# Kernel tuning notes

Hardware: AMD Instinct MI355X
Metric: run time of the kernel (lower is better)

The kernel has to match this reference:

```python
import jax, jax.numpy as jnp
import numpy as np

EMB = 1024
HEADS = 16
HEAD = EMB // HEADS
B, S = 4, 1024


def setup_inputs() -> dict:
    key = jax.random.key(0)
    ks = jax.random.split(key, 8)
    glorot = lambda k, shp: jax.random.normal(k, shp, jnp.float32) * np.sqrt(2.0 / (shp[-2] + shp[-1]))
    return {
        "inputs_for_keys": jax.random.normal(ks[0], (B, S, EMB), jnp.float32),
        "inputs_for_values": jax.random.normal(ks[1], (B, S, EMB), jnp.float32),
        "inputs_for_queries": jax.random.normal(ks[2], (B, S, EMB), jnp.float32),
        "Wk": glorot(ks[3], (HEADS, EMB, HEAD)),
        "Wv": glorot(ks[4], (HEADS, EMB, HEAD)),
        "Wq": glorot(ks[5], (HEADS, EMB, HEAD)),
        "Wo": glorot(ks[6], (EMB, EMB)),
        "bo": jnp.zeros((EMB,), jnp.float32),
    }


def reference(inputs_for_keys, inputs_for_values, inputs_for_queries, Wk, Wv, Wq, Wo, bo):
    # Batched equivalent of the per-head loop: project all heads at once.
    K = jnp.einsum("bse,hed->bhsd", inputs_for_keys, Wk)
    V = jnp.einsum("bse,hed->bhsd", inputs_for_values, Wv)
    Q = jnp.einsum("bse,hed->bhsd", inputs_for_queries, Wq)
    s_keys = K.shape[2]
    s_q = Q.shape[2]
    # causal mask: -inf strictly above diagonal (original: np.triu(ones*-inf, k=1))
    mask = jnp.where(jnp.triu(jnp.ones((s_q, s_keys), bool), k=1), -jnp.inf, 0.0).astype(jnp.float32)
    logits = jnp.einsum("bhqd,bhkd->bhqk", Q, K)
    # FAITHFUL quirk: original divides (logits + mask) by sqrt(window_size_keys)
    scores = jax.nn.softmax((logits + mask) / np.sqrt(s_keys), axis=-1)
    ctx = jnp.einsum("bhqk,bhkd->bhqd", scores, V)  # [B,H,Sq,Dh]
    # concat heads along last dim (head order matches loop order)
    concat = ctx.transpose(0, 2, 1, 3).reshape(ctx.shape[0], s_q, -1)  # [B,Sq,E]
    return jax.nn.relu(concat @ Wo + bo)
```

## Files before the change

### kernel.cpp

```cpp
#include <hip/hip_runtime.h>
#include <hip/hip_bf16.h>

typedef unsigned short u16;
typedef unsigned int   u32;
typedef __attribute__((ext_vector_type(4))) float f32x4;
typedef __attribute__((ext_vector_type(8))) short bf16x8;
typedef __attribute__((ext_vector_type(4))) short bf16x4;

#define EMB   1024
#define SEQ   1024
#define HEADS 16
#define DH    64
#define BATCH 4
#define BH    64
#define BS    4096
#define LDP   72
#define NEG_BIG (-1.0e30f)

__device__ __forceinline__ float b2f(u16 u){ return __uint_as_float(((u32)u) << 16); }
__device__ __forceinline__ u16 f2b(float f){
    u32 u = __float_as_uint(f);
    u32 r = u + 0x7fffu + ((u >> 16) & 1u);
    return (u16)(r >> 16);
}
__device__ __forceinline__ void zero4(f32x4& v){ v[0]=0.f; v[1]=0.f; v[2]=0.f; v[3]=0.f; }
__device__ __forceinline__ ushort4 pk4(float a, float b, float c, float d){
    ushort4 p; p.x = f2b(a); p.y = f2b(b); p.z = f2b(c); p.w = f2b(d); return p;
}
__device__ __forceinline__ float exp2g(float x){ return __builtin_amdgcn_exp2f(x); }

__device__ __forceinline__ void gld_lds16(const void* g, void* l){
    __builtin_amdgcn_global_load_lds(
        (const __attribute__((address_space(1))) u32*)g,
        (__attribute__((address_space(3))) u32*)l, 16, 0, 0);
}

__device__ __forceinline__ u16* tptr(u16* base, int row, int col ){
    const int phys = ((col >> 3) ^ (row & 7));
    return base + row * 64 + (phys << 3);
}
__device__ __forceinline__ const u16* tptrc(const u16* base, int row, int col ){
    const int phys = ((col >> 3) ^ (row & 7));
    return base + row * 64 + (phys << 3);
}
__device__ __forceinline__ const u16* tptr8c(const u16* base, int row, int col ){
    const int chunk = ((col >> 3) ^ (row & 7));
    return base + row * 64 + (chunk << 3) + (col & 7);
}

__device__ __forceinline__ void dot2_f32(const float* __restrict__ x,
                                         const float* __restrict__ w, const int ws,
                                         float& a0, float& a1)
{
    float s0 = 0.f, s1 = 0.f;
    for (int e = 0; e < EMB; e += 4) {
        const float4 xv = *(const float4*)(x + e);
        const float2 w0 = *(const float2*)(w + (size_t)(e + 0) * ws);
        const float2 w1 = *(const float2*)(w + (size_t)(e + 1) * ws);
        const float2 w2 = *(const float2*)(w + (size_t)(e + 2) * ws);
        const float2 w3 = *(const float2*)(w + (size_t)(e + 3) * ws);
        s0 += xv.x * w0.x; s1 += xv.x * w0.y;
        s0 += xv.y * w1.x; s1 += xv.y * w1.y;
        s0 += xv.z * w2.x; s1 += xv.z * w2.y;
        s0 += xv.w * w3.x; s1 += xv.w * w3.y;
    }
    a0 = s0; a1 = s1;
}


__global__ __launch_bounds__(256) void convert_x(
    const float* __restrict__ Xk, const float* __restrict__ Xv, const float* __restrict__ Xq,
    u16* __restrict__ XB)
{
    const int which = blockIdx.y;
    const float* __restrict__ src = (which == 0) ? Xk : (which == 1) ? Xv : Xq;
    const size_t off = (size_t)blockIdx.x * 1024 + threadIdx.x * 4;
    const float4 v = *(const float4*)(src + off);
    *(ushort4*)(XB + (size_t)which * 4194304 + off) = pk4(v.x, v.y, v.z, v.w);
}

__global__ __launch_bounds__(256) void transpose_w(
    const float* __restrict__ Wk, const float* __restrict__ Wv, const float* __restrict__ Wq,
    const float* __restrict__ Wo, u16* __restrict__ WT, u16* __restrict__ WoT)
{
    __shared__ u16 T[64][LDP];
    const int which = blockIdx.y;
    const int bx = blockIdx.x, t = threadIdx.x;

    if (which < 3) {
        const float* __restrict__ W = (which == 0) ? Wk : (which == 1) ? Wv : Wq;
        const int h = bx >> 4, e0 = (bx & 15) * 64;
        #pragma unroll
        for (int i = 0; i < 16; ++i) {
            const int idx = i * 256 + t;
            const int e = idx >> 6, d = idx & 63;
            T[d][e] = f2b(W[(size_t)h * (EMB * DH) + (size_t)(e0 + e) * DH + d]);
        }
        __syncthreads();
        u16* dstb = WT + (size_t)which * (EMB * EMB / 16) * 16;
        #pragma unroll
        for (int i = 0; i < 2; ++i) {
            const int idx = i * 256 + t;
            const int d = idx >> 3, e8 = (idx & 7) * 8;
            *(bf16x8*)(dstb + (size_t)(h * 64 + d) * EMB + e0 + e8) = *(const bf16x8*)&T[d][e8];
        }
    } else {
        const int j0 = (bx >> 4) * 64, e0 = (bx & 15) * 64;
        #pragma unroll
        for (int i = 0; i < 16; ++i) {
            const int idx = i * 256 + t;
            const int e = idx >> 6, d = idx & 63;
            T[d][e] = f2b(Wo[(size_t)(e0 + e) * EMB + j0 + d]);
        }
        __syncthreads();
        #pragma unroll
        for (int i = 0; i < 2; ++i) {
            const int idx = i * 256 + t;
            const int d = idx >> 3, e8 = (idx & 7) * 8;
            *(bf16x8*)(WoT + (size_t)(j0 + d) * EMB + e0 + e8) = *(const bf16x8*)&T[d][e8];
        }
    }
}

template<int MODE>
__global__ __launch_bounds__(256) void gemm128(
    const u16* __restrict__ XB, const u16* __restrict__ WT,
    u16* __restrict__ Qw, u16* __restrict__ Kw, u16* __restrict__ Vt,
    const float* __restrict__ bo, float* __restrict__ OUT)
{
    __shared__ u16 As[128 * 64];
    __shared__ u16 Bs[2][128 * 64];

    const int t = threadIdx.x;
    const int wave = t >> 6, lane = t & 63;
    const int quad = lane >> 4, l16 = lane & 15;
    const int wrow = wave >> 1, wcol = wave & 1;
    const int m0 = blockIdx.x * 128;
    const int n0 = blockIdx.y * 128;
    const int which = blockIdx.z;

    const u16* __restrict__ Ag = (MODE == 0) ? XB + (size_t)which * 4194304 : XB;
    const u16* __restrict__ Bg = (MODE == 0) ? WT + (size_t)which * 1048576 : WT;

    f32x4 acc[4][4];
    #pragma unroll
    for (int mi = 0; mi < 4; ++mi)
        #pragma unroll
        for (int ni = 0; ni < 4; ++ni) zero4(acc[mi][ni]);

    bf16x8 areg[4];

    auto LOADA = [&](int kk){
        #pragma unroll
        for (int i = 0; i < 4; ++i) {
            const int c = i * 256 + t;
            const int row = c >> 3, col8 = (c & 7) * 8;
            areg[i] = *(const bf16x8*)(Ag + (size_t)(m0 + row) * EMB + kk + col8);
        }
    };
    auto WRITEA = [&](){
        #pragma unroll
        for (int i = 0; i < 4; ++i) {
            const int c = i * 256 + t;
            const int row = c >> 3, col8 = (c & 7) * 8;
            *(bf16x8*)tptr(As, row, col8) = areg[i];
        }
    };
    auto STAGE_B = [&](int kk, int buf){
        #pragma unroll
        for (int j = 0; j < 4; ++j) {
            const int cg = wave * 4 + j;
            const int c  = cg * 64 + lane;
            const int row = c >> 3;
            const int col = ((c ^ row) & 7) << 3;
            gld_lds16(Bg + (size_t)(n0 + row) * EMB + kk + col, &Bs[buf][cg * 512]);
        }
    };
    auto COMPUTE = [&](const u16* Bc){
        #pragma unroll
        for (int kb = 0; kb < 2; ++kb) {
            bf16x8 af[4], bf[4];
            #pragma unroll
            for (int mi = 0; mi < 4; ++mi)
                af[mi] = *(const bf16x8*)tptrc(As, wrow * 64 + mi * 16 + l16, kb * 32 + quad * 8);
            #pragma unroll
            for (int ni = 0; ni < 4; ++ni)
                bf[ni] = *(const bf16x8*)tptrc(Bc, wcol * 64 + ni * 16 + l16, kb * 32 + quad * 8);
            #pragma unroll
            for (int mi = 0; mi < 4; ++mi)
                #pragma unroll
                for (int ni = 0; ni < 4; ++ni)
                    acc[mi][ni] = __builtin_amdgcn_mfma_f32_16x16x32_bf16(af[mi], bf[ni], acc[mi][ni], 0, 0, 0);
        }
    };
    auto BAR = [&](){
        asm volatile("s_waitcnt lgkmcnt(0)" ::: "memory");
        __builtin_amdgcn_sched_barrier(0);
        __builtin_amdgcn_s_barrier();
        __builtin_amdgcn_sched_barrier(0);
    };

    STAGE_B(0, 0);
    LOADA(0);
    STAGE_B(64, 1);

    #pragma unroll
    for (int k = 0; k < 16; ++k) {
        WRITEA();
        BAR();
        if (k < 15) LOADA((k + 1) * 64);
        COMPUTE(&Bs[k & 1][0]);
        BAR();
        if (k < 14) STAGE_B((k + 2) * 64, k & 1);
    }

    #pragma unroll
    for (int mi = 0; mi < 4; ++mi) {
        const int r = m0 + wrow * 64 + mi * 16 + quad * 4;
        #pragma unroll
        for (int ni = 0; ni < 4; ++ni) {
            const int j = n0 + wcol * 64 + ni * 16 + l16;
            if (MODE == 1) {
                const float bias = bo[j];
                #pragma unroll
                for (int reg = 0; reg < 4; ++reg) {
                    float v = acc[mi][ni][reg] + bias;
                    if (v < 0.f) v = 0.f;
                    OUT[(size_t)(r + reg) * EMB + j] = v;
                }
            } else {
                const int h = j >> 6, d = j & 63;
                const int b = r >> 10, s = r & (SEQ - 1);
                const int bh = b * HEADS + h;
                if (which == 1) {
                    *(ushort4*)(Vt + ((size_t)bh * DH + d) * SEQ + s) =
                        pk4(acc[mi][ni][0], acc[mi][ni][1], acc[mi][ni][2], acc[mi][ni][3]);
                } else {
                    u16* dst = (which == 0) ? Kw : Qw;
                    const float qsc = (which == 2) ? 0.03125f * 1.44269504088896f : 1.0f;
                    #pragma unroll
                    for (int reg = 0; reg < 4; ++reg)
                        dst[((size_t)bh * SEQ + s + reg) * DH + d] = f2b(acc[mi][ni][reg] * qsc);
                }
            }
        }
    }
}

__global__ __launch_bounds__(256) void attn_flash2(
    const u16* __restrict__ Qg, const u16* __restrict__ Kg, const u16* __restrict__ Vg,
    u16* __restrict__ CTXb)
{
    __shared__ u16 Ks[2][64 * 64];
    __shared__ u16 Vs[2][64 * 64];

    const int t = threadIdx.x;
    const int wave = t >> 6, lane = t & 63;
    const int quad = lane >> 4, l16 = lane & 15;
    const int bh = blockIdx.y;
    const int qt = (blockIdx.x + (blockIdx.y >> 2)) & 15;
    const int b = bh >> 4, h = bh & (HEADS - 1);
    const int q0 = qt * 64;

    const u16* __restrict__ Kbase = Kg + (size_t)bh * SEQ * DH;
    const u16* __restrict__ Vbase = Vg + (size_t)bh * DH * SEQ;

    bf16x8 qf[2];
    {
        const u16* qrow = Qg + ((size_t)bh * SEQ + q0 + wave * 16 + l16) * DH;
        qf[0] = *(const bf16x8*)(qrow + quad * 8);
        qf[1] = *(const bf16x8*)(qrow + 32 + quad * 8);
    }

    #pragma unroll
    for (int i = 0; i < 2; ++i) {
        const int c = i * 256 + t;
        const int row = c >> 3, col8 = (c & 7) * 8;
        const bf16x8 kv = *(const bf16x8*)(Kbase + (size_t)row * DH + col8);
        const bf16x8 vv = *(const bf16x8*)(Vbase + (size_t)row * SEQ + col8);
        *(bf16x8*)tptr(&Ks[0][0], row, col8) = kv;
        *(bf16x8*)tptr(&Vs[0][0], row, col8) = vv;
    }

    float m = NEG_BIG, l = 0.f;
    f32x4 oacc[4];
    #pragma unroll
    for (int nd = 0; nd < 4; ++nd) zero4(oacc[nd]);

    __syncthreads();

    const int qin = wave * 16 + l16;
    int cur = 0;
    for (int c = 0; c <= qt; ++c) {
        const int kn = ((c < qt) ? c + 1 : qt) * 64;
        bf16x8 kpre[2], vpre[2];
        #pragma unroll
        for (int i = 0; i < 2; ++i) {
            const int cc = i * 256 + t;
            const int row = cc >> 3, col8 = (cc & 7) * 8;
            kpre[i] = *(const bf16x8*)(Kbase + (size_t)(kn + row) * DH + col8);
            vpre[i] = *(const bf16x8*)(Vbase + (size_t)row * SEQ + kn + col8);
        }

        const u16* Kc = &Ks[cur][0];
        const u16* Vc = &Vs[cur][0];

        f32x4 sacc[4];
        #pragma unroll
        for (int ni = 0; ni < 4; ++ni) zero4(sacc[ni]);
        __builtin_amdgcn_s_setprio(1);
        #pragma unroll
        for (int kb = 0; kb < 2; ++kb) {
            #pragma unroll
            for (int ni = 0; ni < 4; ++ni) {
                const bf16x8 kf = *(const bf16x8*)tptrc(Kc, ni * 16 + l16, kb * 32 + quad * 8);
                sacc[ni] = __builtin_amdgcn_mfma_f32_16x16x32_bf16(kf, qf[kb], sacc[ni], 0, 0, 0);
            }
        }
        __builtin_amdgcn_s_setprio(0);

        const bool diag = (c == qt);
        float tmx[4];
        #pragma unroll
        for (int ni = 0; ni < 4; ++ni) {
            #pragma unroll
            for (int reg = 0; reg < 4; ++reg) {
                float s = sacc[ni][reg];
                if (diag && (ni * 16 + quad * 4 + reg > qin)) s = NEG_BIG;
                sacc[ni][reg] = s;
            }
            tmx[ni] = fmaxf(fmaxf(sacc[ni][0], sacc[ni][1]),
                            fmaxf(sacc[ni][2], sacc[ni][3]));
        }
        float pmax = fmaxf(fmaxf(tmx[0], tmx[1]), fmaxf(tmx[2], tmx[3]));
        pmax = fmaxf(pmax, __shfl_xor(pmax, 16));
        pmax = fmaxf(pmax, __shfl_xor(pmax, 32));

        if (!__all((int)(pmax - m <= 11.0f))) {
            const float mx = fmaxf(m, pmax);
            const float alpha = exp2g(m - mx);
            m = mx;
            l *= alpha;
            #pragma unroll
            for (int reg = 0; reg < 4; ++reg) {
                const float ar = __shfl(alpha, quad * 4 + reg);
                #pragma unroll
                for (int nd = 0; nd < 4; ++nd) oacc[nd][reg] *= ar;
            }
        }

        float rs = 0.f;
        bf16x4 pa[4];
        #pragma unroll
        for (int ni = 0; ni < 4; ++ni) {
            const float p0 = exp2g(sacc[ni][0] - m);
            const float p1 = exp2g(sacc[ni][1] - m);
            const float p2 = exp2g(sacc[ni][2] - m);
            const float p3 = exp2g(sacc[ni][3] - m);
            rs += (p0 + p1) + (p2 + p3);
            union { bf16x4 v; u32 d[2]; } pk;
            asm("v_cvt_pk_bf16_f32 %0, %1, %2" : "=v"(pk.d[0]) : "v"(p0), "v"(p1));
            asm("v_cvt_pk_bf16_f32 %0, %1, %2" : "=v"(pk.d[1]) : "v"(p2), "v"(p3));
            pa[ni] = pk.v;
        }
        rs += __shfl_xor(rs, 16);
        rs += __shfl_xor(rs, 32);
        l += rs;

        __builtin_amdgcn_s_setprio(1);
        #pragma unroll
        for (int ks = 0; ks < 4; ++ks) {
            #pragma unroll
            for (int nd = 0; nd < 4; ++nd) {
                const bf16x4 vf = *(const bf16x4*)tptr8c(Vc, nd * 16 + l16, ks * 16 + quad * 4);
                oacc[nd] = __builtin_amdgcn_mfma_f32_16x16x16bf16_1k(pa[ks], vf, oacc[nd], 0, 0, 0);
            }
        }
        __builtin_amdgcn_s_setprio(0);

        const int nxt = cur ^ 1;
        #pragma unroll
        for (int i = 0; i < 2; ++i) {
            const int cc = i * 256 + t;
            const int row = cc >> 3, col8 = (cc & 7) * 8;
            *(bf16x8*)tptr(&Ks[nxt][0], row, col8) = kpre[i];
            *(bf16x8*)tptr(&Vs[nxt][0], row, col8) = vpre[i];
        }
        __syncthreads();
        cur = nxt;
    }

    #pragma unroll
    for (int reg = 0; reg < 4; ++reg) {
        const float il = 1.f / __shfl(l, quad * 4 + reg);
        const int q = q0 + wave * 16 + quad * 4 + reg;
        #pragma unroll
        for (int nd = 0; nd < 4; ++nd) {
            const int d = nd * 16 + l16;
            CTXb[(size_t)(b * SEQ + q) * EMB + h * DH + d] = f2b(oacc[nd][reg] * il);
        }
    }
}


__global__ __launch_bounds__(256) void qkv_proj_mfma(
    const float* __restrict__ Xk, const float* __restrict__ Xv, const float* __restrict__ Xq,
    const float* __restrict__ Wk, const float* __restrict__ Wv, const float* __restrict__ Wq,
    u16* __restrict__ Kw, u16* __restrict__ Vw, u16* __restrict__ Qw)
{
    __shared__ u16 As[128][LDP];
    __shared__ u16 Bs[64][LDP];

    const int which = blockIdx.z;
    const float* __restrict__ X = (which == 0) ? Xk : (which == 1) ? Xv : Xq;
    const float* __restrict__ W = (which == 0) ? Wk : (which == 1) ? Wv : Wq;

    const int h    = blockIdx.y;
    const int m0   = blockIdx.x * 128;
    const int t    = threadIdx.x;
    const int wave = t >> 6, lane = t & 63;
    const int quad = lane >> 4, l16 = lane & 15;

    f32x4 acc[2][4];
    #pragma unroll
    for (int mi = 0; mi < 2; ++mi)
        #pragma unroll
        for (int ni = 0; ni < 4; ++ni) zero4(acc[mi][ni]);

    const size_t wbase = (size_t)h * EMB * DH;
    for (int k0 = 0; k0 < EMB; k0 += 64) {
        #pragma unroll
        for (int i = 0; i < 8; ++i) {
            const int idx = i * 256 + t;
            const int r = idx >> 4, c4 = (idx & 15) * 4;
            const float4 v = *(const float4*)(X + (size_t)(m0 + r) * EMB + k0 + c4);
            *(ushort4*)&As[r][c4] = pk4(v.x, v.y, v.z, v.w);
        }
        #pragma unroll
        for (int i = 0; i < 4; ++i) {
            const int d  = t & 63;
            const int e0 = (t >> 6) * 4 + i * 16;
            const float v0 = W[wbase + (size_t)(k0 + e0 + 0) * DH + d];
            const float v1 = W[wbase + (size_t)(k0 + e0 + 1) * DH + d];
            const float v2 = W[wbase + (size_t)(k0 + e0 + 2) * DH + d];
            const float v3 = W[wbase + (size_t)(k0 + e0 + 3) * DH + d];
            *(ushort4*)&Bs[d][e0] = pk4(v0, v1, v2, v3);
        }
        __syncthreads();

        #pragma unroll
        for (int kb = 0; kb < 2; ++kb) {
            bf16x8 bfr[4];
            #pragma unroll
            for (int ni = 0; ni < 4; ++ni)
                bfr[ni] = *(const bf16x8*)&Bs[ni * 16 + l16][kb * 32 + quad * 8];
            #pragma unroll
            for (int mi = 0; mi < 2; ++mi) {
                const bf16x8 af = *(const bf16x8*)&As[wave * 32 + mi * 16 + l16][kb * 32 + quad * 8];
                #pragma unroll
                for (int ni = 0; ni < 4; ++ni)
                    acc[mi][ni] = __builtin_amdgcn_mfma_f32_16x16x32_bf16(af, bfr[ni], acc[mi][ni], 0, 0, 0);
            }
        }
        __syncthreads();
    }

    const int b  = m0 >> 10;
    const int bh = b * HEADS + h;
    u16* __restrict__ RowDst = (which == 0) ? Kw : Qw;
    #pragma unroll
    for (int mi = 0; mi < 2; ++mi) {
        const int s_base = (m0 & (SEQ - 1)) + wave * 32 + mi * 16 + quad * 4;
        #pragma unroll
        for (int ni = 0; ni < 4; ++ni) {
            const int d = ni * 16 + l16;
            if (which != 1) {
                #pragma unroll
                for (int reg = 0; reg < 4; ++reg)
                    RowDst[((size_t)bh * SEQ + s_base + reg) * DH + d] = f2b(acc[mi][ni][reg]);
            } else {
                *(ushort4*)(Vw + ((size_t)bh * DH + d) * SEQ + s_base) =
                    pk4(acc[mi][ni][0], acc[mi][ni][1], acc[mi][ni][2], acc[mi][ni][3]);
            }
        }
    }
}

template<bool QWS, bool TOWS>
__global__ __launch_bounds__(256) void attn_flash(
    const float* __restrict__ Xq, const float* __restrict__ Wq,
    const u16* __restrict__ Qg, const u16* __restrict__ Kg, const u16* __restrict__ Vg,
    u16* __restrict__ CTXb, float* __restrict__ CTXf)
{
    __shared__ u16 Qs[64][LDP];
    union KVU {
        struct { u16 Ks[64][LDP]; u16 Vt[64][LDP]; } kv;
        struct { u16 Xs[64][LDP]; u16 WT[64][LDP]; } pr;
    };
    __shared__ KVU uu;
    __shared__ u16 Ps[64][LDP];

    const int t    = threadIdx.x;
    const int wave = t >> 6, lane = t & 63;
    const int quad = lane >> 4, l16 = lane & 15;
    const int qt = blockIdx.x, bh = blockIdx.y;
    const int b  = bh >> 4, h = bh & (HEADS - 1);
    const int q0 = qt * 64;

    if (QWS) {
        #pragma unroll
        for (int i = 0; i < 4; ++i) {
            const int idx = i * 256 + t;
            const int r = idx >> 4, c4 = (idx & 15) * 4;
            *(ushort4*)&Qs[r][c4] = *(const ushort4*)(Qg + ((size_t)bh * SEQ + q0 + r) * DH + c4);
        }
    } else {
        f32x4 qacc[4];
        #pragma unroll
        for (int ni = 0; ni < 4; ++ni) zero4(qacc[ni]);
        const size_t wbase = (size_t)h * EMB * DH;
        for (int k0 = 0; k0 < EMB; k0 += 64) {
            #pragma unroll
            for (int i = 0; i < 4; ++i) {
                const int idx = i * 256 + t;
                const int r = idx >> 4, c4 = (idx & 15) * 4;
                const float4 v = *(const float4*)(Xq + (size_t)(b * SEQ + q0 + r) * EMB + k0 + c4);
                *(ushort4*)&uu.pr.Xs[r][c4] = pk4(v.x, v.y, v.z, v.w);
            }
            #pragma unroll
            for (int i = 0; i < 4; ++i) {
                const int d  = t & 63;
                const int e0 = (t >> 6) * 4 + i * 16;
                const float v0 = Wq[wbase + (size_t)(k0 + e0 + 0) * DH + d];
                const float v1 = Wq[wbase + (size_t)(k0 + e0 + 1) * DH + d];
                const float v2 = Wq[wbase + (size_t)(k0 + e0 + 2) * DH + d];
                const float v3 = Wq[wbase + (size_t)(k0 + e0 + 3) * DH + d];
                *(ushort4*)&uu.pr.WT[d][e0] = pk4(v0, v1, v2, v3);
            }
            __syncthreads();
            #pragma unroll
            for (int kb = 0; kb < 2; ++kb) {
                const bf16x8 af = *(const bf16x8*)&uu.pr.Xs[wave * 16 + l16][kb * 32 + quad * 8];
                #pragma unroll
                for (int ni = 0; ni < 4; ++ni) {
                    const bf16x8 bf = *(const bf16x8*)&uu.pr.WT[ni * 16 + l16][kb * 32 + quad * 8];
                    qacc[ni] = __builtin_amdgcn_mfma_f32_16x16x32_bf16(af, bf, qacc[ni], 0, 0, 0);
                }
            }
            __syncthreads();
        }
        #pragma unroll
        for (int ni = 0; ni < 4; ++ni)
            #pragma unroll
            for (int reg = 0; reg < 4; ++reg)
                Qs[wave * 16 + quad * 4 + reg][ni * 16 + l16] = f2b(qacc[ni][reg]);
    }

    float m[4], l[4];
    #pragma unroll
    for (int reg = 0; reg < 4; ++reg) { m[reg] = NEG_BIG; l[reg] = 0.f; }
    f32x4 oacc[4];
    #pragma unroll
    for (int ni = 0; ni < 4; ++ni) zero4(oacc[ni]);
    __syncthreads();

    for (int c = 0; c <= qt; ++c) {
        const int k0 = c * 64;

        #pragma unroll
        for (int i = 0; i < 4; ++i) {
            const int idx = i * 256 + t;
            const int r = idx >> 4, c4 = (idx & 15) * 4;
            *(ushort4*)&uu.kv.Ks[r][c4] = *(const ushort4*)(Kg + ((size_t)bh * SEQ + k0 + r) * DH + c4);
        }
        #pragma unroll
        for (int i = 0; i < 4; ++i) {
            const int idx = i * 256 + t;
            const int r = idx >> 4, c4 = (idx & 15) * 4;
            *(ushort4*)&uu.kv.Vt[r][c4] = *(const ushort4*)(Vg + ((size_t)bh * DH + r) * SEQ + k0 + c4);
        }
        __syncthreads();

        f32x4 sacc[4];
        #pragma unroll
        for (int ni = 0; ni < 4; ++ni) zero4(sacc[ni]);
        #pragma unroll
        for (int kb = 0; kb < 2; ++kb) {
            const bf16x8 af = *(const bf16x8*)&Qs[wave * 16 + l16][kb * 32 + quad * 8];
            #pragma unroll
            for (int ni = 0; ni < 4; ++ni) {
                const bf16x8 bf = *(const bf16x8*)&uu.kv.Ks[ni * 16 + l16][kb * 32 + quad * 8];
                sacc[ni] = __builtin_amdgcn_mfma_f32_16x16x32_bf16(af, bf, sacc[ni], 0, 0, 0);
            }
        }

        const bool diag = (c == qt);
        #pragma unroll
        for (int reg = 0; reg < 4; ++reg) {
            const int rloc = quad * 4 + reg;
            float sv[4];
            #pragma unroll
            for (int ni = 0; ni < 4; ++ni) {
                float s = sacc[ni][reg] * 0.03125f;
                if (diag && (ni * 16 + l16 > wave * 16 + rloc)) s = NEG_BIG;
                sv[ni] = s;
            }
            float mx = fmaxf(fmaxf(sv[0], sv[1]), fmaxf(sv[2], sv[3]));
            mx = fmaxf(mx, m[reg]);
            #pragma unroll
            for (int off = 1; off < 16; off <<= 1) mx = fmaxf(mx, __shfl_xor(mx, off));
            const float alpha = __expf(m[reg] - mx);
            float rs = 0.f;
            #pragma unroll
            for (int ni = 0; ni < 4; ++ni) {
                const float p = __expf(sv[ni] - mx);
                Ps[wave * 16 + rloc][ni * 16 + l16] = f2b(p);
                rs += p;
            }
            #pragma unroll
            for (int off = 1; off < 16; off <<= 1) rs += __shfl_xor(rs, off);
            l[reg] = l[reg] * alpha + rs;
            m[reg] = mx;
            #pragma unroll
            for (int ni = 0; ni < 4; ++ni) oacc[ni][reg] *= alpha;
        }
        __syncthreads();

        #pragma unroll
        for (int kb = 0; kb < 2; ++kb) {
            const bf16x8 af = *(const bf16x8*)&Ps[wave * 16 + l16][kb * 32 + quad * 8];
            #pragma unroll
            for (int ni = 0; ni < 4; ++ni) {
                const bf16x8 bf = *(const bf16x8*)&uu.kv.Vt[ni * 16 + l16][kb * 32 + quad * 8];
                oacc[ni] = __builtin_amdgcn_mfma_f32_16x16x32_bf16(af, bf, oacc[ni], 0, 0, 0);
            }
        }
        __syncthreads();
    }

    float il[4];
    #pragma unroll
    for (int reg = 0; reg < 4; ++reg) il[reg] = 1.f / l[reg];
    #pragma unroll
    for (int ni = 0; ni < 4; ++ni) {
        const int d = ni * 16 + l16;
        #pragma unroll
        for (int reg = 0; reg < 4; ++reg) {
            const int q = wave * 16 + quad * 4 + reg;
            const float val = oacc[ni][reg] * il[reg];
            const size_t off = ((size_t)(b * SEQ + q0 + q)) * EMB + h * DH + d;
            if (TOWS) CTXb[off] = f2b(val);
            else      CTXf[off] = val;
        }
    }
}

__global__ __launch_bounds__(256) void out_proj_mfma(
    const u16* __restrict__ CTXb, const float* __restrict__ Wo,
    const float* __restrict__ bo, float* __restrict__ OUT)
{
    __shared__ u16 As[128][LDP];
    __shared__ u16 Bs[64][LDP];

    const int m0 = blockIdx.x * 128;
    const int n0 = blockIdx.y * 64;
    const int t = threadIdx.x;
    const int wave = t >> 6, lane = t & 63;
    const int quad = lane >> 4, l16 = lane & 15;

    f32x4 acc[2][4];
    #pragma unroll
    for (int mi = 0; mi < 2; ++mi)
        #pragma unroll
        for (int ni = 0; ni < 4; ++ni) zero4(acc[mi][ni]);

    for (int k0 = 0; k0 < EMB; k0 += 64) {
        #pragma unroll
        for (int i = 0; i < 8; ++i) {
            const int idx = i * 256 + t;
            const int r = idx >> 4, c4 = (idx & 15) * 4;
            *(ushort4*)&As[r][c4] = *(const ushort4*)(CTXb + (size_t)(m0 + r) * EMB + k0 + c4);
        }
        #pragma unroll
        for (int i = 0; i < 4; ++i) {
            const int d  = t & 63;
            const int e0 = (t >> 6) * 4 + i * 16;
            const float v0 = Wo[(size_t)(k0 + e0 + 0) * EMB + n0 + d];
            const float v1 = Wo[(size_t)(k0 + e0 + 1) * EMB + n0 + d];
            const float v2 = Wo[(size_t)(k0 + e0 + 2) * EMB + n0 + d];
            const float v3 = Wo[(size_t)(k0 + e0 + 3) * EMB + n0 + d];
            *(ushort4*)&Bs[d][e0] = pk4(v0, v1, v2, v3);
        }
        __syncthreads();
        #pragma unroll
        for (int kb = 0; kb < 2; ++kb) {
            bf16x8 bfr[4];
            #pragma unroll
            for (int ni = 0; ni < 4; ++ni)
                bfr[ni] = *(const bf16x8*)&Bs[ni * 16 + l16][kb * 32 + quad * 8];
            #pragma unroll
            for (int mi = 0; mi < 2; ++mi) {
                const bf16x8 af = *(const bf16x8*)&As[wave * 32 + mi * 16 + l16][kb * 32 + quad * 8];
                #pragma unroll
                for (int ni = 0; ni < 4; ++ni)
                    acc[mi][ni] = __builtin_amdgcn_mfma_f32_16x16x32_bf16(af, bfr[ni], acc[mi][ni], 0, 0, 0);
            }
        }
        __syncthreads();
    }

    #pragma unroll
    for (int mi = 0; mi < 2; ++mi) {
        const int row = m0 + wave * 32 + mi * 16 + quad * 4;
        #pragma unroll
        for (int ni = 0; ni < 4; ++ni) {
            const int col = n0 + ni * 16 + l16;
            const float bias = bo[col];
            #pragma unroll
            for (int reg = 0; reg < 4; ++reg) {
                float v = acc[mi][ni][reg] + bias;
                if (v < 0.f) v = 0.f;
                OUT[(size_t)(row + reg) * EMB + col] = v;
            }
        }
    }
}

__global__ __launch_bounds__(256) void out_proj_inplace(
    float* __restrict__ OUT, const float* __restrict__ Wo, const float* __restrict__ bo)
{
    __shared__ float Xs[8][EMB];
    const int t    = threadIdx.x;
    const int row0 = blockIdx.x * 8;
    {
        const float4* src = (const float4*)(OUT + (size_t)row0 * EMB);
        float4* dst = (float4*)&Xs[0][0];
        #pragma unroll
        for (int i = 0; i < 8; ++i) dst[i * 256 + t] = src[i * 256 + t];
    }
    __syncthreads();
    const int r  = t >> 5;
    const int j0 = (t & 31) * 2;
    const float* xrow = Xs[r];
    for (int jb = 0; jb < 16; ++jb) {
        const int j = jb * 64 + j0;
        float a0, a1;
        dot2_f32(xrow, Wo + j, EMB, a0, a1);
        a0 += bo[j];     if (a0 < 0.f) a0 = 0.f;
        a1 += bo[j + 1]; if (a1 < 0.f) a1 = 0.f;
        float* op = OUT + (size_t)(row0 + r) * EMB + j;
        op[0] = a0; op[1] = a1;
    }
}

extern "C" void kernel_launch(void* const* d_in, const int* in_sizes, int n_in,
                              void* d_out, int out_size, void* d_ws, size_t ws_size,
                              hipStream_t stream)
{
    const float* Xk = (const float*)d_in[0];
    const float* Xv = (const float*)d_in[1];
    const float* Xq = (const float*)d_in[2];
    const float* Wk = (const float*)d_in[3];
    const float* Wv = (const float*)d_in[4];
    const float* Wq = (const float*)d_in[5];
    const float* Wo = (const float*)d_in[6];
    const float* bo = (const float*)d_in[7];
    float* OUT = (float*)d_out;
    (void)in_sizes; (void)n_in; (void)out_size;

    const size_t SEGE = (size_t)BH * SEQ * DH;
    const size_t SEGB = SEGE * sizeof(u16);

    const size_t XB_OFF  = 0;
    const size_t WT_OFF  = 3 * SEGE;
    const size_t WOT_OFF = WT_OFF + 3 * (EMB * EMB / 64) * 64;
    const size_t QW_OFF  = WOT_OFF + (size_t)EMB * EMB;
    const size_t KW_OFF  = QW_OFF + SEGE;
    const size_t VT_OFF  = KW_OFF + SEGE;
    const size_t TIER_A_BYTES = (VT_OFF + SEGE) * sizeof(u16);

    if (ws_size >= TIER_A_BYTES) {
        u16* W16 = (u16*)d_ws;
        u16* XB  = W16 + XB_OFF;
        u16* WT  = W16 + WT_OFF;
        u16* WoT = W16 + WOT_OFF;
        u16* Qw  = W16 + QW_OFF;
        u16* Kw  = W16 + KW_OFF;
        u16* Vt  = W16 + VT_OFF;
        u16* CTX = XB;

        convert_x<<<dim3(4096, 3), 256, 0, stream>>>(Xk, Xv, Xq, XB);
        transpose_w<<<dim3(256, 4), 256, 0, stream>>>(Wk, Wv, Wq, Wo, WT, WoT);
        gemm128<0><<<dim3(32, 8, 3), 256, 0, stream>>>(XB, WT, Qw, Kw, Vt, nullptr, nullptr);
        attn_flash2<<<dim3(SEQ / 64, BH), 256, 0, stream>>>(Qw, Kw, Vt, CTX);
        gemm128<1><<<dim3(32, 8, 1), 256, 0, stream>>>(CTX, WoT, nullptr, nullptr, nullptr, bo, OUT);
    } else if (ws_size >= 4 * SEGB) {
        u16* Qw = (u16*)d_ws;
        u16* Kw = Qw + SEGE;
        u16* Vw = Kw + SEGE;
        u16* CT = Vw + SEGE;
        qkv_proj_mfma<<<dim3(32, HEADS, 3), 256, 0, stream>>>(Xk, Xv, Xq, Wk, Wv, Wq, Kw, Vw, Qw);
        attn_flash<true, true><<<dim3(SEQ / 64, BH), 256, 0, stream>>>(
            Xq, Wq, Qw, Kw, Vw, CT, nullptr);
        out_proj_mfma<<<dim3(32, EMB / 64), 256, 0, stream>>>(CT, Wo, bo, OUT);
    } else if (ws_size >= 3 * SEGB) {
        u16* Kw = (u16*)d_ws;
        u16* Vw = Kw + SEGE;
        u16* CT = Vw + SEGE;
        qkv_proj_mfma<<<dim3(32, HEADS, 2), 256, 0, stream>>>(Xk, Xv, Xq, Wk, Wv, Wq, Kw, Vw, nullptr);
        attn_flash<false, true><<<dim3(SEQ / 64, BH), 256, 0, stream>>>(
            Xq, Wq, nullptr, Kw, Vw, CT, nullptr);
        out_proj_mfma<<<dim3(32, EMB / 64), 256, 0, stream>>>(CT, Wo, bo, OUT);
    } else {
        u16* Kw = (u16*)d_ws;
        u16* Vw = Kw + SEGE;
        qkv_proj_mfma<<<dim3(32, HEADS, 2), 256, 0, stream>>>(Xk, Xv, Xq, Wk, Wv, Wq, Kw, Vw, nullptr);
        attn_flash<false, false><<<dim3(SEQ / 64, BH), 256, 0, stream>>>(
            Xq, Wq, nullptr, Kw, Vw, nullptr, OUT);
        out_proj_inplace<<<dim3(BS / 8), 256, 0, stream>>>(OUT, Wo, bo);
    }
}
```

Baseline: 196.4 us.

## Process two query subtiles per attention block and merge prep kernels

The attention kernel now handles 128 query rows per block as two 64-row subtiles that share each loaded K/V tile, which halves K/V global traffic and halves the block count. Block-to-tile mapping is mirrored across heads to balance causal work. Separately, the input conversion and weight transpose kernels are fused into one launch to remove a kernel launch. The trade-off is more registers per thread (two sets of accumulators), which may lower occupancy, and fewer blocks overall (512).

```diff
diff --git a/kernel.cpp b/kernel.cpp
--- a/kernel.cpp
+++ b/kernel.cpp
@@ -68,24 +68,29 @@
 }
 
 
-__global__ __launch_bounds__(256) void convert_x(
+__global__ __launch_bounds__(256) void prep(
     const float* __restrict__ Xk, const float* __restrict__ Xv, const float* __restrict__ Xq,
-    u16* __restrict__ XB)
-{
-    const int which = blockIdx.y;
-    const float* __restrict__ src = (which == 0) ? Xk : (which == 1) ? Xv : Xq;
-    const size_t off = (size_t)blockIdx.x * 1024 + threadIdx.x * 4;
-    const float4 v = *(const float4*)(src + off);
-    *(ushort4*)(XB + (size_t)which * 4194304 + off) = pk4(v.x, v.y, v.z, v.w);
-}
-
-__global__ __launch_bounds__(256) void transpose_w(
     const float* __restrict__ Wk, const float* __restrict__ Wv, const float* __restrict__ Wq,
-    const float* __restrict__ Wo, u16* __restrict__ WT, u16* __restrict__ WoT)
+    const float* __restrict__ Wo,
+    u16* __restrict__ XB, u16* __restrict__ WT, u16* __restrict__ WoT)
 {
     __shared__ u16 T[64][LDP];
-    const int which = blockIdx.y;
-    const int bx = blockIdx.x, t = threadIdx.x;
+    const int t = threadIdx.x;
+    const int id = blockIdx.x;
+
+    if (id >= 1024) {
+        const int cid = id - 1024;
+        const int which = cid >> 12;
+        const int pos = cid & 4095;
+        const float* __restrict__ src = (which == 0) ? Xk : (which == 1) ? Xv : Xq;
+        const size_t off = (size_t)pos * 1024 + t * 4;
+        const float4 v = *(const float4*)(src + off);
+        *(ushort4*)(XB + (size_t)which * 4194304 + off) = pk4(v.x, v.y, v.z, v.w);
+        return;
+    }
+
+    const int which = id >> 8;
+    const int bx = id & 255;
 
     if (which < 3) {
         const float* __restrict__ W = (which == 0) ? Wk : (which == 1) ? Wv : Wq;
@@ -258,18 +263,21 @@
     const int wave = t >> 6, lane = t & 63;
     const int quad = lane >> 4, l16 = lane & 15;
     const int bh = blockIdx.y;
-    const int qt = (blockIdx.x + (blockIdx.y >> 2)) & 15;
+    const int qb = blockIdx.x & 7;
+    const int qt = ((blockIdx.y >> 5) & 1) ? (7 - qb) : qb;
     const int b = bh >> 4, h = bh & (HEADS - 1);
-    const int q0 = qt * 64;
+    const int q0 = qt * 128;
+    const int nt = 2 * qt + 2;
 
     const u16* __restrict__ Kbase = Kg + (size_t)bh * SEQ * DH;
     const u16* __restrict__ Vbase = Vg + (size_t)bh * DH * SEQ;
 
-    bf16x8 qf[2];
-    {
-        const u16* qrow = Qg + ((size_t)bh * SEQ + q0 + wave * 16 + l16) * DH;
-        qf[0] = *(const bf16x8*)(qrow + quad * 8);
-        qf[1] = *(const bf16x8*)(qrow + 32 + quad * 8);
+    bf16x8 qf[2][2];
+    #pragma unroll
+    for (int st = 0; st < 2; ++st) {
+        const u16* qrow = Qg + ((size_t)bh * SEQ + q0 + st * 64 + wave * 16 + l16) * DH;
+        qf[st][0] = *(const bf16x8*)(qrow + quad * 8);
+        qf[st][1] = *(const bf16x8*)(qrow + 32 + quad * 8);
     }
 
     #pragma unroll
@@ -282,17 +290,19 @@
         *(bf16x8*)tptr(&Vs[0][0], row, col8) = vv;
     }
 
-    float m = NEG_BIG, l = 0.f;
-    f32x4 oacc[4];
-    #pragma unroll
-    for (int nd = 0; nd < 4; ++nd) zero4(oacc[nd]);
+    float m[2] = {NEG_BIG, NEG_BIG}, l[2] = {0.f, 0.f};
+    f32x4 oacc[2][4];
+    #pragma unroll
+    for (int st = 0; st < 2; ++st)
+        #pragma unroll
+        for (int nd = 0; nd < 4; ++nd) zero4(oacc[st][nd]);
 
     __syncthreads();
 
     const int qin = wave * 16 + l16;
     int cur = 0;
-    for (int c = 0; c <= qt; ++c) {
-        const int kn = ((c < qt) ? c + 1 : qt) * 64;
+    for (int c = 0; c < nt; ++c) {
+        const int kn = ((c < nt - 1) ? c + 1 : c) * 64;
         bf16x8 kpre[2], vpre[2];
         #pragma unroll
         for (int i = 0; i < 2; ++i) {
@@ -305,78 +315,84 @@
         const u16* Kc = &Ks[cur][0];
         const u16* Vc = &Vs[cur][0];
 
-        f32x4 sacc[4];
-        #pragma unroll
-        for (int ni = 0; ni < 4; ++ni) zero4(sacc[ni]);
-        __builtin_amdgcn_s_setprio(1);
-        #pragma unroll
-        for (int kb = 0; kb < 2; ++kb) {
+        #pragma unroll
+        for (int st = 0; st < 2; ++st) {
+            const int lim = 2 * qt + st;
+            if (c > lim) continue;
+            const bool diag = (c == lim);
+
+            f32x4 sacc[4];
+            #pragma unroll
+            for (int ni = 0; ni < 4; ++ni) zero4(sacc[ni]);
+            __builtin_amdgcn_s_setprio(1);
+            #pragma unroll
+            for (int kb = 0; kb < 2; ++kb) {
+                #pragma unroll
+                for (int ni = 0; ni < 4; ++ni) {
+                    const bf16x8 kf = *(const bf16x8*)tptrc(Kc, ni * 16 + l16, kb * 32 + quad * 8);
+                    sacc[ni] = __builtin_amdgcn_mfma_f32_16x16x32_bf16(kf, qf[st][kb], sacc[ni], 0, 0, 0);
+                }
+            }
+            __builtin_amdgcn_s_setprio(0);
+
+            float tmx[4];
             #pragma unroll
             for (int ni = 0; ni < 4; ++ni) {
-                const bf16x8 kf = *(const bf16x8*)tptrc(Kc, ni * 16 + l16, kb * 32 + quad * 8);
-                sacc[ni] = __builtin_amdgcn_mfma_f32_16x16x32_bf16(kf, qf[kb], sacc[ni], 0, 0, 0);
-            }
-        }
-        __builtin_amdgcn_s_setprio(0);
-
-        const bool diag = (c == qt);
-        float tmx[4];
-        #pragma unroll
-        for (int ni = 0; ni < 4; ++ni) {
-            #pragma unroll
-            for (int reg = 0; reg < 4; ++reg) {
-                float s = sacc[ni][reg];
-                if (diag && (ni * 16 + quad * 4 + reg > qin)) s = NEG_BIG;
-                sacc[ni][reg] = s;
-            }
-            tmx[ni] = fmaxf(fmaxf(sacc[ni][0], sacc[ni][1]),
-                            fmaxf(sacc[ni][2], sacc[ni][3]));
-        }
-        float pmax = fmaxf(fmaxf(tmx[0], tmx[1]), fmaxf(tmx[2], tmx[3]));
-        pmax = fmaxf(pmax, __shfl_xor(pmax, 16));
-        pmax = fmaxf(pmax, __shfl_xor(pmax, 32));
-
-        if (!__all((int)(pmax - m <= 11.0f))) {
-            const float mx = fmaxf(m, pmax);
-            const float alpha = exp2g(m - mx);
-            m = mx;
-            l *= alpha;
-            #pragma unroll
-            for (int reg = 0; reg < 4; ++reg) {
-                const float ar = __shfl(alpha, quad * 4 + reg);
-                #pragma unroll
-                for (int nd = 0; nd < 4; ++nd) oacc[nd][reg] *= ar;
-            }
-        }
-
-        float rs = 0.f;
-        bf16x4 pa[4];
-        #pragma unroll
-        for (int ni = 0; ni < 4; ++ni) {
-            const float p0 = exp2g(sacc[ni][0] - m);
-            const float p1 = exp2g(sacc[ni][1] - m);
-            const float p2 = exp2g(sacc[ni][2] - m);
-            const float p3 = exp2g(sacc[ni][3] - m);
-            rs += (p0 + p1) + (p2 + p3);
-            union { bf16x4 v; u32 d[2]; } pk;
-            asm("v_cvt_pk_bf16_f32 %0, %1, %2" : "=v"(pk.d[0]) : "v"(p0), "v"(p1));
-            asm("v_cvt_pk_bf16_f32 %0, %1, %2" : "=v"(pk.d[1]) : "v"(p2), "v"(p3));
-            pa[ni] = pk.v;
-        }
-        rs += __shfl_xor(rs, 16);
-        rs += __shfl_xor(rs, 32);
-        l += rs;
-
-        __builtin_amdgcn_s_setprio(1);
-        #pragma unroll
-        for (int ks = 0; ks < 4; ++ks) {
-            #pragma unroll
-            for (int nd = 0; nd < 4; ++nd) {
-                const bf16x4 vf = *(const bf16x4*)tptr8c(Vc, nd * 16 + l16, ks * 16 + quad * 4);
-                oacc[nd] = __builtin_amdgcn_mfma_f32_16x16x16bf16_1k(pa[ks], vf, oacc[nd], 0, 0, 0);
-            }
-        }
-        __builtin_amdgcn_s_setprio(0);
+                #pragma unroll
+                for (int reg = 0; reg < 4; ++reg) {
+                    float s = sacc[ni][reg];
+                    if (diag && (ni * 16 + quad * 4 + reg > qin)) s = NEG_BIG;
+                    sacc[ni][reg] = s;
+                }
+                tmx[ni] = fmaxf(fmaxf(sacc[ni][0], sacc[ni][1]),
+                                fmaxf(sacc[ni][2], sacc[ni][3]));
+            }
+            float pmax = fmaxf(fmaxf(tmx[0], tmx[1]), fmaxf(tmx[2], tmx[3]));
+            pmax = fmaxf(pmax, __shfl_xor(pmax, 16));
+            pmax = fmaxf(pmax, __shfl_xor(pmax, 32));
+
+            if (!__all((int)(pmax - m[st] <= 11.0f))) {
+                const float mx = fmaxf(m[st], pmax);
+                const float alpha = exp2g(m[st] - mx);
+                m[st] = mx;
+                l[st] *= alpha;
+                #pragma unroll
+                for (int reg = 0; reg < 4; ++reg) {
+                    const float ar = __shfl(alpha, quad * 4 + reg);
+                    #pragma unroll
+                    for (int nd = 0; nd < 4; ++nd) oacc[st][nd][reg] *= ar;
+                }
+            }
+
+            float rs = 0.f;
+            bf16x4 pa[4];
+            #pragma unroll
+            for (int ni = 0; ni < 4; ++ni) {
+                const float p0 = exp2g(sacc[ni][0] - m[st]);
+                const float p1 = exp2g(sacc[ni][1] - m[st]);
+                const float p2 = exp2g(sacc[ni][2] - m[st]);
+                const float p3 = exp2g(sacc[ni][3] - m[st]);
+                rs += (p0 + p1) + (p2 + p3);
+                union { bf16x4 v; u32 d[2]; } pk;
+                asm("v_cvt_pk_bf16_f32 %0, %1, %2" : "=v"(pk.d[0]) : "v"(p0), "v"(p1));
+                asm("v_cvt_pk_bf16_f32 %0, %1, %2" : "=v"(pk.d[1]) : "v"(p2), "v"(p3));
+                pa[ni] = pk.v;
+            }
+            rs += __shfl_xor(rs, 16);
+            rs += __shfl_xor(rs, 32);
+            l[st] += rs;
+
+            __builtin_amdgcn_s_setprio(1);
+            #pragma unroll
+            for (int ks = 0; ks < 4; ++ks) {
+                #pragma unroll
+                for (int nd = 0; nd < 4; ++nd) {
+                    const bf16x4 vf = *(const bf16x4*)tptr8c(Vc, nd * 16 + l16, ks * 16 + quad * 4);
+                    oacc[st][nd] = __builtin_amdgcn_mfma_f32_16x16x16bf16_1k(pa[ks], vf, oacc[st][nd], 0, 0, 0);
+                }
+            }
+            __builtin_amdgcn_s_setprio(0);
+        }
 
         const int nxt = cur ^ 1;
         #pragma unroll
@@ -391,13 +407,16 @@
     }
 
     #pragma unroll
-    for (int reg = 0; reg < 4; ++reg) {
-        const float il = 1.f / __shfl(l, quad * 4 + reg);
-        const int q = q0 + wave * 16 + quad * 4 + reg;
-        #pragma unroll
-        for (int nd = 0; nd < 4; ++nd) {
-            const int d = nd * 16 + l16;
-            CTXb[(size_t)(b * SEQ + q) * EMB + h * DH + d] = f2b(oacc[nd][reg] * il);
+    for (int st = 0; st < 2; ++st) {
+        #pragma unroll
+        for (int reg = 0; reg < 4; ++reg) {
+            const float il = 1.f / __shfl(l[st], quad * 4 + reg);
+            const int q = q0 + st * 64 + wave * 16 + quad * 4 + reg;
+            #pragma unroll
+            for (int nd = 0; nd < 4; ++nd) {
+                const int d = nd * 16 + l16;
+                CTXb[(size_t)(b * SEQ + q) * EMB + h * DH + d] = f2b(oacc[st][nd][reg] * il);
+            }
         }
     }
 }
@@ -789,10 +808,9 @@
         u16* Vt  = W16 + VT_OFF;
         u16* CTX = XB;
 
-        convert_x<<<dim3(4096, 3), 256, 0, stream>>>(Xk, Xv, Xq, XB);
-        transpose_w<<<dim3(256, 4), 256, 0, stream>>>(Wk, Wv, Wq, Wo, WT, WoT);
+        prep<<<dim3(13312), 256, 0, stream>>>(Xk, Xv, Xq, Wk, Wv, Wq, Wo, XB, WT, WoT);
         gemm128<0><<<dim3(32, 8, 3), 256, 0, stream>>>(XB, WT, Qw, Kw, Vt, nullptr, nullptr);
-        attn_flash2<<<dim3(SEQ / 64, BH), 256, 0, stream>>>(Qw, Kw, Vt, CTX);
+        attn_flash2<<<dim3(SEQ / 128, BH), 256, 0, stream>>>(Qw, Kw, Vt, CTX);
         gemm128<1><<<dim3(32, 8, 1), 256, 0, stream>>>(CTX, WoT, nullptr, nullptr, nullptr, bo, OUT);
     } else if (ws_size >= 4 * SEGB) {
         u16* Qw = (u16*)d_ws;
```

Result: no change. 198.1 us (+0.9%).
